# Performance work log

Hardware: AMD Instinct MI355X
Metric: run time of the kernel (lower is better)

## Reference

```python
import jax, jax.numpy as jnp
import numpy as np

NUM_HEADS = 8

def _ln(x, w, b, eps=1e-5):
    m = x.mean(-1, keepdims=True)
    v = ((x - m) ** 2).mean(-1, keepdims=True)
    return (x - m) / jnp.sqrt(v + eps) * w + b

def _l2n(x, axis=-1, eps=1e-12):
    n = jnp.linalg.norm(x, axis=axis, keepdims=True)
    return x / jnp.maximum(n, eps)

def setup_inputs() -> dict:
    key = jax.random.key(0)
    ks = jax.random.split(key, 30)
    B, N, C, nc, t = 2, 4096, 256, 150, 3
    Hh = Ww = 64
    hid = 4 * C
    s = 0.02
    inp = {}
    inp['x'] = jax.random.normal(ks[0], (B, N, C), jnp.float32)
    inp['z'] = jax.random.normal(ks[1], (B, nc, (t + 1) * N), jnp.float32)
    inp['mem'] = jax.random.normal(ks[2], (B * t, N, C), jnp.float32)
    inp['clustering_w'] = s * jax.random.normal(ks[3], (nc, C), jnp.float32)
    inp['prompt1'] = jax.random.normal(ks[4], (nc,), jnp.float32)
    inp['tdt1'] = jnp.eye(nc, dtype=jnp.float32) + s * jax.random.normal(ks[5], (nc, nc), jnp.float32)
    inp['prompt2'] = jax.random.normal(ks[6], (nc,), jnp.float32)
    inp['tdt2'] = jnp.eye(nc, dtype=jnp.float32) + s * jax.random.normal(ks[7], (nc, nc), jnp.float32)
    inp['sim_alpha'] = jnp.ones((1,), jnp.float32)
    inp['sim_beta'] = jnp.zeros((1,), jnp.float32)
    inp['q_w'] = s * jax.random.normal(ks[8], (C, C), jnp.float32)
    inp['q_b'] = s * jax.random.normal(ks[9], (C,), jnp.float32)
    inp['k_w'] = s * jax.random.normal(ks[10], (C, C), jnp.float32)
    inp['k_b'] = s * jax.random.normal(ks[11], (C,), jnp.float32)
    inp['v_w'] = s * jax.random.normal(ks[12], (C, C), jnp.float32)
    inp['v_b'] = s * jax.random.normal(ks[13], (C,), jnp.float32)
    inp['proj_w'] = s * jax.random.normal(ks[14], (C, C), jnp.float32)
    inp['proj_b'] = s * jax.random.normal(ks[15], (C,), jnp.float32)
    inp['norm_w'] = jnp.ones((C,), jnp.float32)
    inp['norm_b'] = jnp.zeros((C,), jnp.float32)
    inp['fc1_w'] = s * jax.random.normal(ks[16], (hid, C), jnp.float32)
    inp['fc1_b'] = s * jax.random.normal(ks[17], (hid,), jnp.float32)
    inp['dw_w'] = s * jax.random.normal(ks[18], (hid, 1, 3, 3), jnp.float32)
    inp['dw_b'] = s * jax.random.normal(ks[19], (hid,), jnp.float32)
    inp['fc2_w'] = s * jax.random.normal(ks[20], (C, hid), jnp.float32)
    inp['fc2_b'] = s * jax.random.normal(ks[21], (C,), jnp.float32)
    inp['H'] = Hh
    inp['W'] = Ww
    inp['t'] = t
    return inp

def _forward(x, z, mem, clustering_w, prompt1, tdt1, prompt2, tdt2, sim_alpha, sim_beta,
             q_w, q_b, k_w, k_b, v_w, v_b, proj_w, proj_b, norm_w, norm_b,
             fc1_w, fc1_b, dw_w, dw_b, fc2_w, fc2_b, H, W, t):
    B, N, C = x.shape
    nc = clustering_w.shape[0]
    res = x
    T = t + 1
    # cat memory frames with current frame: [(B*T), N, C]
    xf = jnp.concatenate([mem.reshape(B, t, N, C), x[:, None]], axis=1).reshape(B * T, N, C)
    # clustering head: (SRPS approximated as identity) 1x1 conv dim->num_clusters
    cl = jnp.einsum('bnc,kc->bkn', xf, clustering_w)            # [(B*T), nc, N]
    cl = cl.reshape(B, T, nc, N).transpose(0, 2, 1, 3).reshape(B, nc, T * N)
    # top-down prompt modulation of z and cluster logits
    zc = z.transpose(0, 2, 1)                                   # [B, T*N, nc]
    cos = _l2n(zc, -1) @ _l2n(prompt1[None, :, None], axis=1)   # [B, T*N, 1]
    zc = (zc * jnp.clip(cos, 0.0, 1.0)) @ tdt1
    clc = cl.transpose(0, 2, 1)
    cos = _l2n(clc, -1) @ _l2n(prompt2[None, :, None], axis=1)
    clc = (clc * jnp.clip(cos, 0.0, 1.0)) @ tdt2
    cluster_x_z = ((clc + zc) * 0.5).transpose(0, 2, 1)          # [B, nc, T*N]
    # inner_center: per-frame soft assignment -> cluster centers
    center = cluster_x_z.reshape(B, nc, T, N).transpose(0, 2, 1, 3)  # [B, T, nc, N]
    assigned_results = center
    soft = jax.nn.softmax(center, axis=-1)
    cx = xf.reshape(B, T, N, C)
    cen = jnp.einsum('btkn,btnc->btkc', soft, cx)               # [B, T, nc, C]
    last, prev = cen[:, -1], cen[:, :-1]                        # [B,nc,C], [B,t,nc,C]
    dot = jnp.einsum('bkc,btkc->btk', last, prev)
    denom = jnp.maximum(jnp.linalg.norm(last, axis=-1)[:, None] * jnp.linalg.norm(prev, axis=-1), 1e-8)
    gate = jax.nn.sigmoid(sim_beta + sim_alpha * (dot / denom))  # [B, t, nc]
    C_in = last + (gate[..., None] * prev).sum(axis=1)          # [B, nc, C]
    C_in = _ln(C_in, norm_w, norm_b)
    # cross attention: tokens query cluster centers
    hd = C // NUM_HEADS
    q = (res @ q_w.T + q_b) * (1.0 / np.sqrt(hd))
    k = C_in @ k_w.T + k_b
    v = C_in @ v_w.T + v_b
    q = q.reshape(B, N, NUM_HEADS, hd).transpose(0, 2, 1, 3)
    k = k.reshape(B, nc, NUM_HEADS, hd).transpose(0, 2, 1, 3)
    v = v.reshape(B, nc, NUM_HEADS, hd).transpose(0, 2, 1, 3)
    attn = jax.nn.softmax(jnp.einsum('bhnd,bhkd->bhnk', q, k), axis=-1)
    o = jnp.einsum('bhnk,bhkd->bhnd', attn, v).transpose(0, 2, 1, 3).reshape(B, N, C)
    o = o @ proj_w.T + proj_b
    out = res + _ln(o, norm_w, norm_b)
    # MLP with depthwise conv
    h = out @ fc1_w.T + fc1_b                                   # [B, N, 4C]
    hid = h.shape[-1]
    h_img = h.transpose(0, 2, 1).reshape(B, hid, H, W)
    h_img = jax.lax.conv_general_dilated(h_img, dw_w, (1, 1), 'SAME',
                                         feature_group_count=hid,
                                         dimension_numbers=('NCHW', 'OIHW', 'NCHW'))
    h_img = h_img + dw_b[None, :, None, None]
    h = h_img.reshape(B, hid, N).transpose(0, 2, 1)
    h = jax.nn.gelu(h, approximate=False) @ fc2_w.T + fc2_b
    out = out + _ln(h, norm_w, norm_b)
    return out, cluster_x_z, assigned_results

def reference(x, z, mem, clustering_w, prompt1, tdt1, prompt2, tdt2, sim_alpha, sim_beta,
              q_w, q_b, k_w, k_b, v_w, v_b, proj_w, proj_b, norm_w, norm_b,
              fc1_w, fc1_b, dw_w, dw_b, fc2_w, fc2_b, H, W, t):
    return _forward(x, z, mem, clustering_w, prompt1, tdt1, prompt2, tdt2, sim_alpha, sim_beta,
                    q_w, q_b, k_w, k_b, v_w, v_b, proj_w, proj_b, norm_w, norm_b,
                    fc1_w, fc1_b, dw_w, dw_b, fc2_w, fc2_b, H, W, t)
```

## Files before the change

### kernel.cpp

```cpp
#include <hip/hip_runtime.h>
#include <math.h>


typedef __attribute__((ext_vector_type(8))) short bf16x8;
typedef __attribute__((ext_vector_type(4))) float f32x4;

__device__ __forceinline__ short f2b(float f) {
  union { float f; unsigned int u; } c; c.f = f;
  unsigned int r = (c.u + 0x7fffu + ((c.u >> 16) & 1u)) >> 16;
  return (short)r;
}

__device__ __forceinline__ float bred_sum(float v, float* red) {
  int tid = threadIdx.x;
  red[tid] = v; __syncthreads();
  #pragma unroll
  for (int s = 128; s > 0; s >>= 1) {
    if (tid < s) red[tid] += red[tid + s];
    __syncthreads();
  }
  float r = red[0]; __syncthreads();
  return r;
}

__global__ __launch_bounds__(256) void gemm_mfma(
    const float* __restrict__ A, const float* __restrict__ W,
    const float* __restrict__ bias, float* __restrict__ out,
    int M, int N, int K, float alpha)
{
  __shared__ __align__(16) short As[128 * 72];
  __shared__ __align__(16) short Bs[64 * 72];
  const int tid = threadIdx.x;
  const int m0 = blockIdx.x * 128;
  const int n0 = blockIdx.y * 64;
  const int wave = tid >> 6;
  const int lane = tid & 63;
  const int wm = wave & 1, wn = wave >> 1;
  const int t16 = lane & 15;
  const int k8 = (lane >> 4) * 8;

  f32x4 acc[4][2];
  #pragma unroll
  for (int i = 0; i < 4; ++i)
    #pragma unroll
    for (int j = 0; j < 2; ++j)
      acc[i][j] = (f32x4){0.f, 0.f, 0.f, 0.f};

  const int sr = tid >> 2;
  const int sk = (tid & 3) * 16;

  for (int k0 = 0; k0 < K; k0 += 64) {
    #pragma unroll
    for (int p = 0; p < 2; ++p) {
      const int row = sr + p * 64;
      const float* ap = &A[(size_t)(m0 + row) * K + k0 + sk];
      float4 v0 = *(const float4*)&ap[0];
      float4 v1 = *(const float4*)&ap[4];
      float4 v2 = *(const float4*)&ap[8];
      float4 v3 = *(const float4*)&ap[12];
      bf16x8 w0, w1;
      w0[0] = f2b(v0.x); w0[1] = f2b(v0.y); w0[2] = f2b(v0.z); w0[3] = f2b(v0.w);
      w0[4] = f2b(v1.x); w0[5] = f2b(v1.y); w0[6] = f2b(v1.z); w0[7] = f2b(v1.w);
      w1[0] = f2b(v2.x); w1[1] = f2b(v2.y); w1[2] = f2b(v2.z); w1[3] = f2b(v2.w);
      w1[4] = f2b(v3.x); w1[5] = f2b(v3.y); w1[6] = f2b(v3.z); w1[7] = f2b(v3.w);
      *(bf16x8*)&As[row * 72 + sk] = w0;
      *(bf16x8*)&As[row * 72 + sk + 8] = w1;
    }
    {
      const float* wp = &W[(size_t)(n0 + sr) * K + k0 + sk];
      float4 v0 = *(const float4*)&wp[0];
      float4 v1 = *(const float4*)&wp[4];
      float4 v2 = *(const float4*)&wp[8];
      float4 v3 = *(const float4*)&wp[12];
      bf16x8 w0, w1;
      w0[0] = f2b(v0.x); w0[1] = f2b(v0.y); w0[2] = f2b(v0.z); w0[3] = f2b(v0.w);
      w0[4] = f2b(v1.x); w0[5] = f2b(v1.y); w0[6] = f2b(v1.z); w0[7] = f2b(v1.w);
      w1[0] = f2b(v2.x); w1[1] = f2b(v2.y); w1[2] = f2b(v2.z); w1[3] = f2b(v2.w);
      w1[4] = f2b(v3.x); w1[5] = f2b(v3.y); w1[6] = f2b(v3.z); w1[7] = f2b(v3.w);
      *(bf16x8*)&Bs[sr * 72 + sk] = w0;
      *(bf16x8*)&Bs[sr * 72 + sk + 8] = w1;
    }
    __syncthreads();
    #pragma unroll
    for (int ks = 0; ks < 2; ++ks) {
      const int kofs = ks * 32 + k8;
      bf16x8 af0 = *(const bf16x8*)&As[(wm * 64 +  0 + t16) * 72 + kofs];
      bf16x8 af1 = *(const bf16x8*)&As[(wm * 64 + 16 + t16) * 72 + kofs];
      bf16x8 af2 = *(const bf16x8*)&As[(wm * 64 + 32 + t16) * 72 + kofs];
      bf16x8 af3 = *(const bf16x8*)&As[(wm * 64 + 48 + t16) * 72 + kofs];
      bf16x8 bf0 = *(const bf16x8*)&Bs[(wn * 32 +  0 + t16) * 72 + kofs];
      bf16x8 bf1 = *(const bf16x8*)&Bs[(wn * 32 + 16 + t16) * 72 + kofs];
      acc[0][0] = __builtin_amdgcn_mfma_f32_16x16x32_bf16(af0, bf0, acc[0][0], 0, 0, 0);
      acc[1][0] = __builtin_amdgcn_mfma_f32_16x16x32_bf16(af1, bf0, acc[1][0], 0, 0, 0);
      acc[2][0] = __builtin_amdgcn_mfma_f32_16x16x32_bf16(af2, bf0, acc[2][0], 0, 0, 0);
      acc[3][0] = __builtin_amdgcn_mfma_f32_16x16x32_bf16(af3, bf0, acc[3][0], 0, 0, 0);
      acc[0][1] = __builtin_amdgcn_mfma_f32_16x16x32_bf16(af0, bf1, acc[0][1], 0, 0, 0);
      acc[1][1] = __builtin_amdgcn_mfma_f32_16x16x32_bf16(af1, bf1, acc[1][1], 0, 0, 0);
      acc[2][1] = __builtin_amdgcn_mfma_f32_16x16x32_bf16(af2, bf1, acc[2][1], 0, 0, 0);
      acc[3][1] = __builtin_amdgcn_mfma_f32_16x16x32_bf16(af3, bf1, acc[3][1], 0, 0, 0);
    }
    __syncthreads();
  }
  const int r4 = (lane >> 4) * 4;
  #pragma unroll
  for (int ni = 0; ni < 2; ++ni) {
    const int gcol = n0 + wn * 32 + ni * 16 + t16;
    const float bb = bias[gcol];
    #pragma unroll
    for (int mi = 0; mi < 4; ++mi) {
      #pragma unroll
      for (int r = 0; r < 4; ++r) {
        const int gm = m0 + wm * 64 + mi * 16 + r4 + r;
        out[(size_t)gm * N + gcol] = alpha * (acc[mi][ni][r] + bb);
      }
    }
  }
}

__global__ __launch_bounds__(256) void gemm_cl_mfma(
    const float* __restrict__ x, const float* __restrict__ mem,
    const float* __restrict__ cw, float* __restrict__ clr)
{
  __shared__ __align__(16) short As[128 * 72];
  __shared__ __align__(16) short Bs[64 * 72];
  const int tid = threadIdx.x;
  const int m0 = blockIdx.x * 128;
  const int n0 = blockIdx.y * 64;
  const int bt = m0 >> 12;
  const int b = bt >> 2, ti = bt & 3;
  const int nbase = m0 & 4095;
  const float* Abase = (ti < 3) ? (mem + (size_t)(b * 3 + ti) * 4096 * 256)
                                : (x + (size_t)b * 4096 * 256);
  const int wave = tid >> 6, lane = tid & 63;
  const int wm = wave & 1, wn = wave >> 1;
  const int t16 = lane & 15;
  const int k8 = (lane >> 4) * 8;

  f32x4 acc[4][2];
  #pragma unroll
  for (int i = 0; i < 4; ++i)
    #pragma unroll
    for (int j = 0; j < 2; ++j)
      acc[i][j] = (f32x4){0.f, 0.f, 0.f, 0.f};

  const int sr = tid >> 2;
  const int sk = (tid & 3) * 16;

  for (int k0 = 0; k0 < 256; k0 += 64) {
    #pragma unroll
    for (int p = 0; p < 2; ++p) {
      const int row = sr + p * 64;
      const float* ap = &Abase[(size_t)(nbase + row) * 256 + k0 + sk];
      float4 v0 = *(const float4*)&ap[0];
      float4 v1 = *(const float4*)&ap[4];
      float4 v2 = *(const float4*)&ap[8];
      float4 v3 = *(const float4*)&ap[12];
      bf16x8 w0, w1;
      w0[0] = f2b(v0.x); w0[1] = f2b(v0.y); w0[2] = f2b(v0.z); w0[3] = f2b(v0.w);
      w0[4] = f2b(v1.x); w0[5] = f2b(v1.y); w0[6] = f2b(v1.z); w0[7] = f2b(v1.w);
      w1[0] = f2b(v2.x); w1[1] = f2b(v2.y); w1[2] = f2b(v2.z); w1[3] = f2b(v2.w);
      w1[4] = f2b(v3.x); w1[5] = f2b(v3.y); w1[6] = f2b(v3.z); w1[7] = f2b(v3.w);
      *(bf16x8*)&As[row * 72 + sk] = w0;
      *(bf16x8*)&As[row * 72 + sk + 8] = w1;
    }
    {
      const int gn = n0 + sr;
      bf16x8 w0 = {0,0,0,0,0,0,0,0}, w1 = {0,0,0,0,0,0,0,0};
      if (gn < 150) {
        const float* wp = &cw[(size_t)gn * 256 + k0 + sk];
        float4 v0 = *(const float4*)&wp[0];
        float4 v1 = *(const float4*)&wp[4];
        float4 v2 = *(const float4*)&wp[8];
        float4 v3 = *(const float4*)&wp[12];
        w0[0] = f2b(v0.x); w0[1] = f2b(v0.y); w0[2] = f2b(v0.z); w0[3] = f2b(v0.w);
        w0[4] = f2b(v1.x); w0[5] = f2b(v1.y); w0[6] = f2b(v1.z); w0[7] = f2b(v1.w);
        w1[0] = f2b(v2.x); w1[1] = f2b(v2.y); w1[2] = f2b(v2.z); w1[3] = f2b(v2.w);
        w1[4] = f2b(v3.x); w1[5] = f2b(v3.y); w1[6] = f2b(v3.z); w1[7] = f2b(v3.w);
      }
      *(bf16x8*)&Bs[sr * 72 + sk] = w0;
      *(bf16x8*)&Bs[sr * 72 + sk + 8] = w1;
    }
    __syncthreads();
    #pragma unroll
    for (int ks = 0; ks < 2; ++ks) {
      const int kofs = ks * 32 + k8;
      bf16x8 af0 = *(const bf16x8*)&As[(wm * 64 +  0 + t16) * 72 + kofs];
      bf16x8 af1 = *(const bf16x8*)&As[(wm * 64 + 16 + t16) * 72 + kofs];
      bf16x8 af2 = *(const bf16x8*)&As[(wm * 64 + 32 + t16) * 72 + kofs];
      bf16x8 af3 = *(const bf16x8*)&As[(wm * 64 + 48 + t16) * 72 + kofs];
      bf16x8 bf0 = *(const bf16x8*)&Bs[(wn * 32 +  0 + t16) * 72 + kofs];
      bf16x8 bf1 = *(const bf16x8*)&Bs[(wn * 32 + 16 + t16) * 72 + kofs];
      acc[0][0] = __builtin_amdgcn_mfma_f32_16x16x32_bf16(af0, bf0, acc[0][0], 0, 0, 0);
      acc[1][0] = __builtin_amdgcn_mfma_f32_16x16x32_bf16(af1, bf0, acc[1][0], 0, 0, 0);
      acc[2][0] = __builtin_amdgcn_mfma_f32_16x16x32_bf16(af2, bf0, acc[2][0], 0, 0, 0);
      acc[3][0] = __builtin_amdgcn_mfma_f32_16x16x32_bf16(af3, bf0, acc[3][0], 0, 0, 0);
      acc[0][1] = __builtin_amdgcn_mfma_f32_16x16x32_bf16(af0, bf1, acc[0][1], 0, 0, 0);
      acc[1][1] = __builtin_amdgcn_mfma_f32_16x16x32_bf16(af1, bf1, acc[1][1], 0, 0, 0);
      acc[2][1] = __builtin_amdgcn_mfma_f32_16x16x32_bf16(af2, bf1, acc[2][1], 0, 0, 0);
      acc[3][1] = __builtin_amdgcn_mfma_f32_16x16x32_bf16(af3, bf1, acc[3][1], 0, 0, 0);
    }
    __syncthreads();
  }
  const int r4 = (lane >> 4) * 4;
  const size_t rowbase = (size_t)b * 16384 + ti * 4096 + nbase;
  #pragma unroll
  for (int ni = 0; ni < 2; ++ni) {
    const int col = n0 + wn * 32 + ni * 16 + t16;
    if (col >= 160) continue;
    #pragma unroll
    for (int mi = 0; mi < 4; ++mi) {
      const int mrow = wm * 64 + mi * 16 + r4;
      #pragma unroll
      for (int r = 0; r < 4; ++r)
        clr[(rowbase + mrow + r) * 160 + col] = acc[mi][ni][r];
    }
  }
}

__global__ __launch_bounds__(256) void cos_stats(
    const float* __restrict__ z, const float* __restrict__ clr,
    const float* __restrict__ p1, const float* __restrict__ p2,
    float* __restrict__ cosz, float* __restrict__ coscl)
{
  int which = blockIdx.y;
  int gid = blockIdx.x * 256 + threadIdx.x;
  int b = gid >> 14, m = gid & 16383;
  float d = 0, s = 0, pn = 0;
  if (which) {
    const float* sp = clr + ((size_t)b * 16384 + m) * 160;
    for (int k = 0; k < 148; k += 4) {
      float4 v = *(const float4*)&sp[k];
      float4 a = *(const float4*)&p2[k];
      d += v.x * a.x + v.y * a.y + v.z * a.z + v.w * a.w;
      s += v.x * v.x + v.y * v.y + v.z * v.z + v.w * v.w;
      pn += a.x * a.x + a.y * a.y + a.z * a.z + a.w * a.w;
    }
    for (int k = 148; k < 150; ++k) {
      float v = sp[k], a = p2[k];
      d += v * a; s += v * v; pn += a * a;
    }
    float c = d / (fmaxf(sqrtf(s), 1e-12f) * fmaxf(sqrtf(pn), 1e-12f));
    coscl[gid] = fminf(fmaxf(c, 0.f), 1.f);
  } else {
    const float* sp = z + (size_t)b * 150 * 16384 + m;
    for (int k = 0; k < 150; ++k) {
      float v = sp[(size_t)k * 16384];
      float a = p1[k];
      d += v * a; s += v * v; pn += a * a;
    }
    float c = d / (fmaxf(sqrtf(s), 1e-12f) * fmaxf(sqrtf(pn), 1e-12f));
    cosz[gid] = fminf(fmaxf(c, 0.f), 1.f);
  }
}

__global__ __launch_bounds__(256) void gemm_csz_mfma(
    const float* __restrict__ clr, const float* __restrict__ z,
    const float* __restrict__ coscl, const float* __restrict__ cosz,
    const float* __restrict__ tdt2, const float* __restrict__ tdt1,
    float* __restrict__ csz, float* __restrict__ asg)
{
  __shared__ __align__(16) short As[128 * 40];
  __shared__ __align__(16) short Bs[64 * 40];
  const int tid = threadIdx.x;
  const int m0 = blockIdx.x * 128;
  const int b = m0 >> 14;
  const int mm = m0 & 16383;
  const int n0 = blockIdx.y * 64;
  const int wave = tid >> 6, lane = tid & 63;
  const int wm = wave & 1, wn = wave >> 1;
  const int t16 = lane & 15;
  const int k8 = (lane >> 4) * 8;

  f32x4 acc[4][2];
  #pragma unroll
  for (int i = 0; i < 4; ++i)
    #pragma unroll
    for (int j = 0; j < 2; ++j)
      acc[i][j] = (f32x4){0.f, 0.f, 0.f, 0.f};

  for (int c = 0; c < 10; ++c) {
    if (c < 5) {
      const int row = tid >> 1;
      const int sk0 = (tid & 1) * 16;
      const float* ap = &clr[((size_t)b * 16384 + mm + row) * 160 + c * 32 + sk0];
      const float cs = coscl[(size_t)b * 16384 + mm + row];
      float4 v0 = *(const float4*)&ap[0];
      float4 v1 = *(const float4*)&ap[4];
      float4 v2 = *(const float4*)&ap[8];
      float4 v3 = *(const float4*)&ap[12];
      bf16x8 w0, w1;
      w0[0] = f2b(v0.x * cs); w0[1] = f2b(v0.y * cs); w0[2] = f2b(v0.z * cs); w0[3] = f2b(v0.w * cs);
      w0[4] = f2b(v1.x * cs); w0[5] = f2b(v1.y * cs); w0[6] = f2b(v1.z * cs); w0[7] = f2b(v1.w * cs);
      w1[0] = f2b(v2.x * cs); w1[1] = f2b(v2.y * cs); w1[2] = f2b(v2.z * cs); w1[3] = f2b(v2.w * cs);
      w1[4] = f2b(v3.x * cs); w1[5] = f2b(v3.y * cs); w1[6] = f2b(v3.z * cs); w1[7] = f2b(v3.w * cs);
      *(bf16x8*)&As[row * 40 + sk0] = w0;
      *(bf16x8*)&As[row * 40 + sk0 + 8] = w1;
    } else {
      const int kgl = tid >> 3;
      const int mb = (tid & 7) * 4;
      const int kg = (c - 5) * 32 + kgl;
      #pragma unroll
      for (int p = 0; p < 4; ++p) {
        const int m = mb + p * 32;
        float4 v = make_float4(0.f, 0.f, 0.f, 0.f);
        if (kg < 150) {
          v = *(const float4*)&z[((size_t)b * 150 + kg) * 16384 + mm + m];
          float4 cz = *(const float4*)&cosz[(size_t)b * 16384 + mm + m];
          v.x *= cz.x; v.y *= cz.y; v.z *= cz.z; v.w *= cz.w;
        }
        As[(m + 0) * 40 + kgl] = f2b(v.x);
        As[(m + 1) * 40 + kgl] = f2b(v.y);
        As[(m + 2) * 40 + kgl] = f2b(v.z);
        As[(m + 3) * 40 + kgl] = f2b(v.w);
      }
    }
    {
      const int kc = tid & 63;
      const int gn = n0 + kc;
      #pragma unroll
      for (int p = 0; p < 8; ++p) {
        const int kgl = (tid >> 6) + p * 4;
        const int kg = c * 32 + kgl;
        float t = 0.f;
        if (gn < 150) {
          if (kg < 150) t = tdt2[kg * 150 + gn];
          else if (kg >= 160 && kg < 310) t = tdt1[(kg - 160) * 150 + gn];
        }
        Bs[kc * 40 + kgl] = f2b(t);
      }
    }
    __syncthreads();
    {
      bf16x8 af0 = *(const bf16x8*)&As[(wm * 64 +  0 + t16) * 40 + k8];
      bf16x8 af1 = *(const bf16x8*)&As[(wm * 64 + 16 + t16) * 40 + k8];
      bf16x8 af2 = *(const bf16x8*)&As[(wm * 64 + 32 + t16) * 40 + k8];
      bf16x8 af3 = *(const bf16x8*)&As[(wm * 64 + 48 + t16) * 40 + k8];
      bf16x8 bf0 = *(const bf16x8*)&Bs[(wn * 32 +  0 + t16) * 40 + k8];
      bf16x8 bf1 = *(const bf16x8*)&Bs[(wn * 32 + 16 + t16) * 40 + k8];
      acc[0][0] = __builtin_amdgcn_mfma_f32_16x16x32_bf16(af0, bf0, acc[0][0], 0, 0, 0);
      acc[1][0] = __builtin_amdgcn_mfma_f32_16x16x32_bf16(af1, bf0, acc[1][0], 0, 0, 0);
      acc[2][0] = __builtin_amdgcn_mfma_f32_16x16x32_bf16(af2, bf0, acc[2][0], 0, 0, 0);
      acc[3][0] = __builtin_amdgcn_mfma_f32_16x16x32_bf16(af3, bf0, acc[3][0], 0, 0, 0);
      acc[0][1] = __builtin_amdgcn_mfma_f32_16x16x32_bf16(af0, bf1, acc[0][1], 0, 0, 0);
      acc[1][1] = __builtin_amdgcn_mfma_f32_16x16x32_bf16(af1, bf1, acc[1][1], 0, 0, 0);
      acc[2][1] = __builtin_amdgcn_mfma_f32_16x16x32_bf16(af2, bf1, acc[2][1], 0, 0, 0);
      acc[3][1] = __builtin_amdgcn_mfma_f32_16x16x32_bf16(af3, bf1, acc[3][1], 0, 0, 0);
    }
    __syncthreads();
  }
  const int r4 = (lane >> 4) * 4;
  const int ti = mm >> 12;
  const int nn = mm & 4095;
  #pragma unroll
  for (int ni = 0; ni < 2; ++ni) {
    const int kc = n0 + wn * 32 + ni * 16 + t16;
    if (kc >= 150) continue;
    #pragma unroll
    for (int mi = 0; mi < 4; ++mi) {
      const int mrow = wm * 64 + mi * 16 + r4;
      float4 r;
      r.x = 0.5f * acc[mi][ni][0];
      r.y = 0.5f * acc[mi][ni][1];
      r.z = 0.5f * acc[mi][ni][2];
      r.w = 0.5f * acc[mi][ni][3];
      *(float4*)&csz[((size_t)b * 150 + kc) * 16384 + mm + mrow] = r;
      *(float4*)&asg[(((size_t)b * 4 + ti) * 150 + kc) * 4096 + nn + mrow] = r;
    }
  }
}

__global__ __launch_bounds__(256) void softmax_stats_e(
    const float* __restrict__ csz, float* __restrict__ lr_, short* __restrict__ ecsz)
{
  __shared__ float wred[8];
  const int row = blockIdx.x;
  const int bt = row / 150, k = row - bt * 150;
  const int b = bt >> 2, ti = bt & 3;
  const float* p = csz + ((size_t)b * 150 + k) * 16384 + ti * 4096;
  const int base = threadIdx.x * 16;
  float4 v[4];
  #pragma unroll
  for (int i = 0; i < 4; ++i) v[i] = *(const float4*)&p[base + i * 4];
  float mx = -1e30f;
  #pragma unroll
  for (int i = 0; i < 4; ++i)
    mx = fmaxf(mx, fmaxf(fmaxf(v[i].x, v[i].y), fmaxf(v[i].z, v[i].w)));
  #pragma unroll
  for (int off = 1; off < 64; off <<= 1) mx = fmaxf(mx, __shfl_xor(mx, off));
  const int wave = threadIdx.x >> 6, lane = threadIdx.x & 63;
  if (lane == 0) wred[wave] = mx;
  __syncthreads();
  mx = fmaxf(fmaxf(wred[0], wred[1]), fmaxf(wred[2], wred[3]));
  const float L = 1.4426950408889634f;
  float s = 0.f;
  bf16x8 e0, e1;
  #pragma unroll
  for (int i = 0; i < 2; ++i) {
    float a = exp2f((v[i].x - mx) * L);
    float bq = exp2f((v[i].y - mx) * L);
    float cq = exp2f((v[i].z - mx) * L);
    float dq = exp2f((v[i].w - mx) * L);
    s += a + bq + cq + dq;
    e0[i * 4 + 0] = f2b(a); e0[i * 4 + 1] = f2b(bq); e0[i * 4 + 2] = f2b(cq); e0[i * 4 + 3] = f2b(dq);
  }
  #pragma unroll
  for (int i = 2; i < 4; ++i) {
    float a = exp2f((v[i].x - mx) * L);
    float bq = exp2f((v[i].y - mx) * L);
    float cq = exp2f((v[i].z - mx) * L);
    float dq = exp2f((v[i].w - mx) * L);
    s += a + bq + cq + dq;
    e1[(i - 2) * 4 + 0] = f2b(a); e1[(i - 2) * 4 + 1] = f2b(bq);
    e1[(i - 2) * 4 + 2] = f2b(cq); e1[(i - 2) * 4 + 3] = f2b(dq);
  }
  #pragma unroll
  for (int off = 1; off < 64; off <<= 1) s += __shfl_xor(s, off);
  if (lane == 0) wred[4 + wave] = s;
  __syncthreads();
  short* er = ecsz + ((size_t)bt * 160 + k) * 4096 + base;
  *(bf16x8*)&er[0] = e0;
  *(bf16x8*)&er[8] = e1;
  if (threadIdx.x == 0) lr_[row] = wred[4] + wred[5] + wred[6] + wred[7];
}

__global__ __launch_bounds__(256) void gemm_cen_at(
    const short* __restrict__ ecsz, const float* __restrict__ x, const float* __restrict__ mem,
    float* __restrict__ cen)
{
  __shared__ __align__(16) short As[160 * 136];
  const int tid = threadIdx.x;
  const int chalf = blockIdx.x;
  const int bt = blockIdx.y;
  const int sp = blockIdx.z;
  const int b = bt >> 2, ti = bt & 3;
  const float* xf = (ti < 3) ? (mem + (size_t)(b * 3 + ti) * 4096 * 256)
                             : (x + (size_t)b * 4096 * 256);
  const int n0 = sp * 256;
  const int wave = tid >> 6, lane = tid & 63;
  const int t16 = lane & 15, quad = lane >> 4, k8 = quad * 8;
  const int cbase = chalf * 128 + wave * 32;

  f32x4 acc[10][2];
  #pragma unroll
  for (int i = 0; i < 10; ++i) {
    acc[i][0] = (f32x4){0.f, 0.f, 0.f, 0.f};
    acc[i][1] = (f32x4){0.f, 0.f, 0.f, 0.f};
  }

  const short* erow = ecsz + (size_t)bt * 160 * 4096 + n0;
  #pragma unroll
  for (int half = 0; half < 2; ++half) {
    #pragma unroll
    for (int p = 0; p < 10; ++p) {
      const int g = p * 256 + tid;
      const int row = g >> 4;
      const int col8 = (g & 15) * 8;
      *(bf16x8*)&As[row * 136 + col8] =
          *(const bf16x8*)&erow[(size_t)row * 4096 + half * 128 + col8];
    }
    __syncthreads();
    #pragma unroll
    for (int kc = 0; kc < 4; ++kc) {
      bf16x8 bB[2];
      #pragma unroll
      for (int nt = 0; nt < 2; ++nt) {
        bf16x8 w;
        #pragma unroll
        for (int j = 0; j < 8; ++j)
          w[j] = f2b(xf[(size_t)(n0 + half * 128 + kc * 32 + k8 + j) * 256 + cbase + nt * 16 + t16]);
        bB[nt] = w;
      }
      #pragma unroll
      for (int mt = 0; mt < 10; ++mt) {
        bf16x8 aA = *(const bf16x8*)&As[(mt * 16 + t16) * 136 + kc * 32 + k8];
        acc[mt][0] = __builtin_amdgcn_mfma_f32_16x16x32_bf16(aA, bB[0], acc[mt][0], 0, 0, 0);
        acc[mt][1] = __builtin_amdgcn_mfma_f32_16x16x32_bf16(aA, bB[1], acc[mt][1], 0, 0, 0);
      }
    }
    __syncthreads();
  }
  #pragma unroll
  for (int mt = 0; mt < 10; ++mt) {
    #pragma unroll
    for (int r = 0; r < 4; ++r) {
      const int grow = mt * 16 + quad * 4 + r;
      if (grow < 150) {
        atomicAdd(&cen[((size_t)bt * 150 + grow) * 256 + cbase + t16], acc[mt][0][r]);
        atomicAdd(&cen[((size_t)bt * 150 + grow) * 256 + cbase + 16 + t16], acc[mt][1][r]);
      }
    }
  }
}

__global__ __launch_bounds__(256) void gate_ln(
    const float* __restrict__ cen, const float* __restrict__ lr_,
    const float* __restrict__ alpha_, const float* __restrict__ beta_,
    const float* __restrict__ nw, const float* __restrict__ nb, float* __restrict__ cin)
{
  __shared__ float red[256];
  int bk = blockIdx.x;
  int b = bk / 150, k = bk % 150;
  int c = threadIdx.x;
  const float* base = cen + ((size_t)b * 4 * 150) * 256;
  const float* lrb = lr_ + (size_t)b * 4 * 150;
  float lc  = base[((size_t)3 * 150 + k) * 256 + c] / lrb[3 * 150 + k];
  float p0  = base[((size_t)0 * 150 + k) * 256 + c] / lrb[0 * 150 + k];
  float p1v = base[((size_t)1 * 150 + k) * 256 + c] / lrb[1 * 150 + k];
  float p2v = base[((size_t)2 * 150 + k) * 256 + c] / lrb[2 * 150 + k];
  float nl = bred_sum(lc * lc, red);
  float q0 = bred_sum(p0 * p0, red);
  float q1 = bred_sum(p1v * p1v, red);
  float q2 = bred_sum(p2v * p2v, red);
  float d0 = bred_sum(lc * p0, red);
  float d1 = bred_sum(lc * p1v, red);
  float d2 = bred_sum(lc * p2v, red);
  float al = alpha_[0], be = beta_[0];
  float snl = sqrtf(nl);
  float g0 = 1.f / (1.f + expf(-(be + al * (d0 / fmaxf(snl * sqrtf(q0), 1e-8f)))));
  float g1 = 1.f / (1.f + expf(-(be + al * (d1 / fmaxf(snl * sqrtf(q1), 1e-8f)))));
// ... 149 lines not shown
      ls += __shfl_xor(ls, 4);
      ls += __shfl_xor(ls, 8);
      if (t16 == 0) lrow[wr + mt * 16 + quad * 4 + r] = 1.f / ls;
      #pragma unroll
      for (int ct = 0; ct < 10; ++ct)
        Ps[(wr + mt * 16 + quad * 4 + r) * 168 + ct * 16 + t16] = f2b(s[mt][ct][r]);
    }
  }
  __syncthreads();

  f32x4 oacc[2][2];
  #pragma unroll
  for (int i = 0; i < 2; ++i)
    #pragma unroll
    for (int j = 0; j < 2; ++j)
      oacc[i][j] = (f32x4){0.f, 0.f, 0.f, 0.f};
  #pragma unroll
  for (int kstep = 0; kstep < 5; ++kstep) {
    bf16x8 bV0 = *(const bf16x8*)&VT[( 0 + t16) * 168 + kstep * 32 + k8];
    bf16x8 bV1 = *(const bf16x8*)&VT[(16 + t16) * 168 + kstep * 32 + k8];
    #pragma unroll
    for (int mt = 0; mt < 2; ++mt) {
      bf16x8 aP = *(const bf16x8*)&Ps[(wr + mt * 16 + t16) * 168 + kstep * 32 + k8];
      oacc[mt][0] = __builtin_amdgcn_mfma_f32_16x16x32_bf16(aP, bV0, oacc[mt][0], 0, 0, 0);
      oacc[mt][1] = __builtin_amdgcn_mfma_f32_16x16x32_bf16(aP, bV1, oacc[mt][1], 0, 0, 0);
    }
  }
  #pragma unroll
  for (int mt = 0; mt < 2; ++mt) {
    #pragma unroll
    for (int nt = 0; nt < 2; ++nt) {
      const int d = nt * 16 + t16;
      #pragma unroll
      for (int r = 0; r < 4; ++r) {
        const int row = wr + mt * 16 + quad * 4 + r;
        o[((size_t)b * 4096 + n0 + row) * 256 + h * 32 + d] = oacc[mt][nt][r] * lrow[row];
      }
    }
  }
}

__global__ __launch_bounds__(256) void ln_res(
    const float* __restrict__ src, const float* __restrict__ res,
    const float* __restrict__ nw, const float* __restrict__ nb, float* __restrict__ dst)
{
  const int wave = threadIdx.x >> 6;
  const int lane = threadIdx.x & 63;
  const size_t row = (size_t)blockIdx.x * 4 + wave;
  const int c = lane * 4;
  float4 v = *(const float4*)&src[row * 256 + c];
  float s  = v.x + v.y + v.z + v.w;
  float s2 = v.x * v.x + v.y * v.y + v.z * v.z + v.w * v.w;
  #pragma unroll
  for (int off = 1; off < 64; off <<= 1) {
    s  += __shfl_xor(s, off);
    s2 += __shfl_xor(s2, off);
  }
  const float mu = s * (1.f / 256.f);
  const float var = s2 * (1.f / 256.f) - mu * mu;
  const float inv = rsqrtf(var + 1e-5f);
  float4 w = *(const float4*)&nw[c];
  float4 bb = *(const float4*)&nb[c];
  float4 rr = *(const float4*)&res[row * 256 + c];
  float4 d;
  d.x = rr.x + (v.x - mu) * inv * w.x + bb.x;
  d.y = rr.y + (v.y - mu) * inv * w.y + bb.y;
  d.z = rr.z + (v.z - mu) * inv * w.z + bb.z;
  d.w = rr.w + (v.w - mu) * inv * w.w + bb.w;
  *(float4*)&dst[row * 256 + c] = d;
}

__global__ __launch_bounds__(256) void conv_wt(
    const float* __restrict__ w, float* __restrict__ wt)
{
  int i = blockIdx.x * 256 + threadIdx.x;
  if (i < 9216) {
    int ch = i / 9, tap = i - ch * 9;
    wt[tap * 1024 + ch] = w[i];
  }
}

__global__ __launch_bounds__(256) void conv_gelu(
    const float* __restrict__ h, const float* __restrict__ wt, const float* __restrict__ bias,
    float* __restrict__ hc)
{
  const int pix = blockIdx.x;
  const int b = pix >> 12;
  const int n = pix & 4095;
  const int y = n >> 6, xx = n & 63;
  const int c4 = threadIdx.x * 4;
  float4 acc = *(const float4*)&bias[c4];
  const float* hb = h + ((size_t)b * 4096) * 1024 + c4;
  #pragma unroll
  for (int dy = 0; dy < 3; ++dy) {
    const int yy = y + dy - 1;
    if (yy < 0 || yy > 63) continue;
    #pragma unroll
    for (int dx = 0; dx < 3; ++dx) {
      const int xv = xx + dx - 1;
      if (xv < 0 || xv > 63) continue;
      float4 hv = *(const float4*)&hb[(size_t)(yy * 64 + xv) * 1024];
      float4 wv = *(const float4*)&wt[(dy * 3 + dx) * 1024 + c4];
      acc.x = fmaf(hv.x, wv.x, acc.x);
      acc.y = fmaf(hv.y, wv.y, acc.y);
      acc.z = fmaf(hv.z, wv.z, acc.z);
      acc.w = fmaf(hv.w, wv.w, acc.w);
    }
  }
  float4 g;
  g.x = 0.5f * acc.x * (1.f + erff(acc.x * 0.70710678118654752f));
  g.y = 0.5f * acc.y * (1.f + erff(acc.y * 0.70710678118654752f));
  g.z = 0.5f * acc.z * (1.f + erff(acc.z * 0.70710678118654752f));
  g.w = 0.5f * acc.w * (1.f + erff(acc.w * 0.70710678118654752f));
  *(float4*)&hc[((size_t)b * 4096 + n) * 1024 + c4] = g;
}

extern "C" void kernel_launch(void* const* d_in, const int* in_sizes, int n_in,
                              void* d_out, int out_size, void* d_ws, size_t ws_size,
                              hipStream_t stream)
{
  (void)in_sizes; (void)n_in; (void)out_size; (void)ws_size;
  const float* x    = (const float*)d_in[0];
  const float* z    = (const float*)d_in[1];
  const float* mem  = (const float*)d_in[2];
  const float* cw   = (const float*)d_in[3];
  const float* p1   = (const float*)d_in[4];
  const float* tdt1 = (const float*)d_in[5];
  const float* p2   = (const float*)d_in[6];
  const float* tdt2 = (const float*)d_in[7];
  const float* sal  = (const float*)d_in[8];
  const float* sbe  = (const float*)d_in[9];
  const float* q_w  = (const float*)d_in[10];
  const float* q_b  = (const float*)d_in[11];
  const float* k_w  = (const float*)d_in[12];
  const float* k_b  = (const float*)d_in[13];
  const float* v_w  = (const float*)d_in[14];
  const float* v_b  = (const float*)d_in[15];
  const float* pj_w = (const float*)d_in[16];
  const float* pj_b = (const float*)d_in[17];
  const float* nw   = (const float*)d_in[18];
  const float* nb   = (const float*)d_in[19];
  const float* f1w  = (const float*)d_in[20];
  const float* f1b  = (const float*)d_in[21];
  const float* dww  = (const float*)d_in[22];
  const float* dwb  = (const float*)d_in[23];
  const float* f2w  = (const float*)d_in[24];
  const float* f2b_ = (const float*)d_in[25];

  float* out = (float*)d_out;
  float* csz = out + 2097152;
  float* asg = csz + 4915200;

  float* ws    = (float*)d_ws;
  float* clr   = ws;
  short* ecsz  = (short*)ws;
  float* coscl = ws + 5242880;
  float* cosz  = ws + 5275648;
  float* lr_   = ws + 5308416;
  float* cen   = ws + 5310816;
  float* cin   = ws + 5618016;
  float* q     = ws + 5694816;
  float* ksb   = ws + 7791968;
  float* vsb   = ws + 7868768;
  float* o     = ws + 7945568;
  float* h     = ws;
  float* hc    = ws + 8388608;
  float* tmp   = ws + 16777216;
  float* out1  = ws + 18874368;
  float* wt    = ws + 20971520;

  dim3 blk(256);
  gemm_cl_mfma<<<dim3(256, 3), blk, 0, stream>>>(x, mem, cw, clr);
  cos_stats<<<dim3(128, 2), blk, 0, stream>>>(z, clr, p1, p2, cosz, coscl);
  gemm_csz_mfma<<<dim3(256, 3), blk, 0, stream>>>(clr, z, coscl, cosz, tdt2, tdt1, csz, asg);
  softmax_stats_e<<<dim3(1200), blk, 0, stream>>>(csz, lr_, ecsz);
  hipMemsetAsync(cen, 0, (size_t)1200 * 256 * sizeof(float), stream);
  gemm_cen_at<<<dim3(2, 8, 16), blk, 0, stream>>>(ecsz, x, mem, cen);
  gate_ln<<<dim3(300), blk, 0, stream>>>(cen, lr_, sal, sbe, nw, nb, cin);
  gemm_mfma<<<dim3(64, 4), blk, 0, stream>>>(x, q_w, q_b, q, 8192, 256, 256, 0.17677669529663687f);
  gemm_nt<<<dim3(3, 4), blk, 0, stream>>>(cin, k_w, k_b, ksb, 300, 256, 256, 1.f);
  gemm_nt<<<dim3(3, 4), blk, 0, stream>>>(cin, v_w, v_b, vsb, 300, 256, 256, 1.f);
  attn_mfma<<<dim3(512), blk, 0, stream>>>(q, ksb, vsb, o);
  gemm_mfma<<<dim3(64, 4), blk, 0, stream>>>(o, pj_w, pj_b, tmp, 8192, 256, 256, 1.f);
  ln_res<<<dim3(2048), blk, 0, stream>>>(tmp, x, nw, nb, out1);
  gemm_mfma<<<dim3(64, 16), blk, 0, stream>>>(out1, f1w, f1b, h, 8192, 1024, 256, 1.f);
  conv_wt<<<dim3(36), blk, 0, stream>>>(dww, wt);
  conv_gelu<<<dim3(8192), blk, 0, stream>>>(h, wt, dwb, hc);
  gemm_mfma<<<dim3(64, 4), blk, 0, stream>>>(hc, f2w, f2b_, tmp, 8192, 256, 1024, 1.f);
  ln_res<<<dim3(2048), blk, 0, stream>>>(tmp, out1, nw, nb, out);
}
```

Measured before the change: 447.9 us.

## Fuse clustering GEMM with cosine gating into a bf16 concatenated operand

After: 445.5 us. No clear change (-0.5%).

```diff
diff --git a/kernel.cpp b/kernel.cpp
--- a/kernel.cpp
+++ b/kernel.cpp
@@ -117,254 +117,227 @@
   }
 }
 
-__global__ __launch_bounds__(256) void gemm_cl_mfma(
+__global__ __launch_bounds__(256) void prep_bt(
+    const float* __restrict__ cw, const float* __restrict__ tdt2, const float* __restrict__ tdt1,
+    short* __restrict__ cwb, short* __restrict__ TT)
+{
+  int idx = blockIdx.x * 256 + threadIdx.x;
+  if (idx < 160 * 256) {
+    int kc = idx >> 8, k = idx & 255;
+    float v = (kc < 150) ? cw[kc * 256 + k] : 0.f;
+    cwb[idx] = f2b(v);
+  }
+  if (idx < 160 * 320) {
+    int kc = idx / 320, kk = idx - kc * 320;
+    float t = 0.f;
+    if (kc < 150) {
+      if (kk < 150) t = tdt2[kk * 150 + kc];
+      else if (kk >= 160 && kk < 310) t = tdt1[(kk - 160) * 150 + kc];
+    }
+    TT[idx] = f2b(t);
+  }
+}
+
+__global__ __launch_bounds__(256) void cl_cos_prep(
     const float* __restrict__ x, const float* __restrict__ mem,
-    const float* __restrict__ cw, float* __restrict__ clr)
-{
-  __shared__ __align__(16) short As[128 * 72];
-  __shared__ __align__(16) short Bs[64 * 72];
+    const short* __restrict__ cwb, const float* __restrict__ p2,
+    short* __restrict__ Acat)
+{
+  __shared__ __align__(16) short ls[64][168];
+  __shared__ float p2s[160];
   const int tid = threadIdx.x;
-  const int m0 = blockIdx.x * 128;
-  const int n0 = blockIdx.y * 64;
-  const int bt = m0 >> 12;
-  const int b = bt >> 2, ti = bt & 3;
-  const int nbase = m0 & 4095;
-  const float* Abase = (ti < 3) ? (mem + (size_t)(b * 3 + ti) * 4096 * 256)
-                                : (x + (size_t)b * 4096 * 256);
+  const int r0 = blockIdx.x * 64;
+  const int b = r0 >> 14, ti = (r0 >> 12) & 3;
+  const int nn0 = r0 & 4095;
+  const float* Ab = ((ti < 3) ? (mem + (size_t)(b * 3 + ti) * 4096 * 256)
+                              : (x + (size_t)b * 4096 * 256)) + (size_t)nn0 * 256;
+  const int wave = tid >> 6, lane = tid & 63;
+  const int t16 = lane & 15, quad = lane >> 4, k8 = quad * 8;
+  if (tid < 160) p2s[tid] = (tid < 150) ? p2[tid] : 0.f;
+  __syncthreads();
+
+  f32x4 acc[10];
+  #pragma unroll
+  for (int i = 0; i < 10; ++i) acc[i] = (f32x4){0.f, 0.f, 0.f, 0.f};
+  const float* ap = Ab + (size_t)(wave * 16 + t16) * 256 + k8;
+  const short* bp = cwb + t16 * 256 + k8;
+  #pragma unroll 2
+  for (int ks = 0; ks < 8; ++ks) {
+    float4 v0 = *(const float4*)&ap[ks * 32];
+    float4 v1 = *(const float4*)&ap[ks * 32 + 4];
+    bf16x8 a;
+    a[0] = f2b(v0.x); a[1] = f2b(v0.y); a[2] = f2b(v0.z); a[3] = f2b(v0.w);
+    a[4] = f2b(v1.x); a[5] = f2b(v1.y); a[6] = f2b(v1.z); a[7] = f2b(v1.w);
+    #pragma unroll
+    for (int nf = 0; nf < 10; ++nf) {
+      bf16x8 bv = *(const bf16x8*)&bp[nf * 4096 + ks * 32];
+      acc[nf] = __builtin_amdgcn_mfma_f32_16x16x32_bf16(a, bv, acc[nf], 0, 0, 0);
+    }
+  }
+  float d[4] = {0.f, 0.f, 0.f, 0.f}, s[4] = {0.f, 0.f, 0.f, 0.f};
+  float pn = 0.f;
+  #pragma unroll
+  for (int nf = 0; nf < 10; ++nf) {
+    float a2 = p2s[nf * 16 + t16];
+    pn += a2 * a2;
+    #pragma unroll
+    for (int r = 0; r < 4; ++r) {
+      float v = acc[nf][r];
+      d[r] = fmaf(v, a2, d[r]);
+      s[r] = fmaf(v, v, s[r]);
+    }
+  }
+  #pragma unroll
+  for (int off = 1; off < 16; off <<= 1) {
+    pn += __shfl_xor(pn, off);
+    #pragma unroll
+    for (int r = 0; r < 4; ++r) {
+      d[r] += __shfl_xor(d[r], off);
+      s[r] += __shfl_xor(s[r], off);
+    }
+  }
+  const float spn = fmaxf(sqrtf(pn), 1e-12f);
+  float cs[4];
+  #pragma unroll
+  for (int r = 0; r < 4; ++r) {
+    float c = d[r] / (fmaxf(sqrtf(s[r]), 1e-12f) * spn);
+    cs[r] = fminf(fmaxf(c, 0.f), 1.f);
+  }
+  #pragma unroll
+  for (int nf = 0; nf < 10; ++nf)
+    #pragma unroll
+    for (int r = 0; r < 4; ++r)
+      ls[wave * 16 + quad * 4 + r][nf * 16 + t16] = f2b(acc[nf][r] * cs[r]);
+  __syncthreads();
+  #pragma unroll
+  for (int i = 0; i < 5; ++i) {
+    const int idx = tid + i * 256;
+    const int m = idx / 20, seg = idx - m * 20;
+    *(bf16x8*)&Acat[(size_t)(r0 + m) * 320 + seg * 8] = *(const bf16x8*)&ls[m][seg * 8];
+  }
+}
+
+__global__ __launch_bounds__(256) void z_prep(
+    const float* __restrict__ z, const float* __restrict__ p1, short* __restrict__ Acat)
+{
+  __shared__ __align__(16) float zs[160][68];
+  __shared__ float sred[4][16][9];
+  __shared__ float czs[64];
+  const int tid = threadIdx.x;
+  const int C0 = blockIdx.x * 64;
+  const int b = C0 >> 14;
+  const int mmb = C0 & 16383;
+  const int kr = tid >> 4, c4 = (tid & 15) * 4;
+  float d[4] = {0.f, 0.f, 0.f, 0.f}, sv[4] = {0.f, 0.f, 0.f, 0.f};
+  float pn = 0.f;
+  #pragma unroll
+  for (int it = 0; it < 10; ++it) {
+    const int k = it * 16 + kr;
+    float4 v = make_float4(0.f, 0.f, 0.f, 0.f);
+    float a = 0.f;
+    if (k < 150) {
+      v = *(const float4*)&z[((size_t)b * 150 + k) * 16384 + mmb + c4];
+      a = p1[k];
+    }
+    *(float4*)&zs[k][c4] = v;
+    d[0] = fmaf(v.x, a, d[0]); d[1] = fmaf(v.y, a, d[1]);
+    d[2] = fmaf(v.z, a, d[2]); d[3] = fmaf(v.w, a, d[3]);
+    sv[0] = fmaf(v.x, v.x, sv[0]); sv[1] = fmaf(v.y, v.y, sv[1]);
+    sv[2] = fmaf(v.z, v.z, sv[2]); sv[3] = fmaf(v.w, v.w, sv[3]);
+    pn = fmaf(a, a, pn);
+  }
+  const int lane = tid & 63, wave = tid >> 6;
+  #pragma unroll
+  for (int off = 16; off < 64; off <<= 1) {
+    pn += __shfl_xor(pn, off);
+    #pragma unroll
+    for (int r = 0; r < 4; ++r) {
+      d[r] += __shfl_xor(d[r], off);
+      sv[r] += __shfl_xor(sv[r], off);
+    }
+  }
+  if ((lane >> 4) == 0) {
+    #pragma unroll
+    for (int r = 0; r < 4; ++r) {
+      sred[wave][lane][r] = d[r];
+      sred[wave][lane][4 + r] = sv[r];
+    }
+    sred[wave][lane][8] = pn;
+  }
+  __syncthreads();
+  if (tid < 64) {
+    const int cg = tid >> 2, r = tid & 3;
+    float dd = 0.f, ss = 0.f, pp = 0.f;
+    #pragma unroll
+    for (int w = 0; w < 4; ++w) {
+      dd += sred[w][cg][r];
+      ss += sred[w][cg][4 + r];
+      pp += sred[w][cg][8];
+    }
+    float c = dd / (fmaxf(sqrtf(ss), 1e-12f) * fmaxf(sqrtf(pp), 1e-12f));
+    czs[tid] = fminf(fmaxf(c, 0.f), 1.f);
+  }
+  __syncthreads();
+  #pragma unroll
+  for (int i = 0; i < 5; ++i) {
+    const int idx = tid + i * 256;
+    const int m = idx / 20, seg = idx - m * 20;
+    const float cz = czs[m];
+    bf16x8 w;
+    #pragma unroll
+    for (int j = 0; j < 8; ++j) w[j] = f2b(zs[seg * 8 + j][m] * cz);
+    *(bf16x8*)&Acat[(size_t)(C0 + m) * 320 + 160 + seg * 8] = w;
+  }
+}
+
+__global__ __launch_bounds__(256) void gemm_csz2(
+    const short* __restrict__ Acat, const short* __restrict__ TT,
+    float* __restrict__ csz, float* __restrict__ asg)
+{
+  const int tid = threadIdx.x;
+  const int r0 = blockIdx.x * 64;
+  const int b = r0 >> 14;
+  const int mmg = r0 & 16383;
+  const int ti = mmg >> 12, nn = mmg & 4095;
   const int wave = tid >> 6, lane = tid & 63;
   const int wm = wave & 1, wn = wave >> 1;
-  const int t16 = lane & 15;
-  const int k8 = (lane >> 4) * 8;
-
-  f32x4 acc[4][2];
-  #pragma unroll
-  for (int i = 0; i < 4; ++i)
-    #pragma unroll
-    for (int j = 0; j < 2; ++j)
+  const int t16 = lane & 15, quad = lane >> 4, k8 = quad * 8;
+  f32x4 acc[2][5];
+  #pragma unroll
+  for (int i = 0; i < 2; ++i)
+    #pragma unroll
+    for (int j = 0; j < 5; ++j)
       acc[i][j] = (f32x4){0.f, 0.f, 0.f, 0.f};
 
-  const int sr = tid >> 2;
-  const int sk = (tid & 3) * 16;
-
-  for (int k0 = 0; k0 < 256; k0 += 64) {
-    #pragma unroll
-    for (int p = 0; p < 2; ++p) {
-      const int row = sr + p * 64;
-      const float* ap = &Abase[(size_t)(nbase + row) * 256 + k0 + sk];
-      float4 v0 = *(const float4*)&ap[0];
-      float4 v1 = *(const float4*)&ap[4];
-      float4 v2 = *(const float4*)&ap[8];
-      float4 v3 = *(const float4*)&ap[12];
-      bf16x8 w0, w1;
-      w0[0] = f2b(v0.x); w0[1] = f2b(v0.y); w0[2] = f2b(v0.z); w0[3] = f2b(v0.w);
-      w0[4] = f2b(v1.x); w0[5] = f2b(v1.y); w0[6] = f2b(v1.z); w0[7] = f2b(v1.w);
-      w1[0] = f2b(v2.x); w1[1] = f2b(v2.y); w1[2] = f2b(v2.z); w1[3] = f2b(v2.w);
-      w1[4] = f2b(v3.x); w1[5] = f2b(v3.y); w1[6] = f2b(v3.z); w1[7] = f2b(v3.w);
-      *(bf16x8*)&As[row * 72 + sk] = w0;
-      *(bf16x8*)&As[row * 72 + sk + 8] = w1;
-    }
-    {
-      const int gn = n0 + sr;
-      bf16x8 w0 = {0,0,0,0,0,0,0,0}, w1 = {0,0,0,0,0,0,0,0};
-      if (gn < 150) {
-        const float* wp = &cw[(size_t)gn * 256 + k0 + sk];
-        float4 v0 = *(const float4*)&wp[0];
-        float4 v1 = *(const float4*)&wp[4];
-        float4 v2 = *(const float4*)&wp[8];
-        float4 v3 = *(const float4*)&wp[12];
-        w0[0] = f2b(v0.x); w0[1] = f2b(v0.y); w0[2] = f2b(v0.z); w0[3] = f2b(v0.w);
-        w0[4] = f2b(v1.x); w0[5] = f2b(v1.y); w0[6] = f2b(v1.z); w0[7] = f2b(v1.w);
-        w1[0] = f2b(v2.x); w1[1] = f2b(v2.y); w1[2] = f2b(v2.z); w1[3] = f2b(v2.w);
-        w1[4] = f2b(v3.x); w1[5] = f2b(v3.y); w1[6] = f2b(v3.z); w1[7] = f2b(v3.w);
+  const short* a0p = Acat + (size_t)(r0 + wm * 32 + t16) * 320 + k8;
+  const short* a1p = a0p + 16 * 320;
+  const short* bp  = TT + (size_t)(wn * 80 + t16) * 320 + k8;
+  #pragma unroll 2
+  for (int ks = 0; ks < 10; ++ks) {
+    bf16x8 a0 = *(const bf16x8*)&a0p[ks * 32];
+    bf16x8 a1 = *(const bf16x8*)&a1p[ks * 32];
+    #pragma unroll
+    for (int nf = 0; nf < 5; ++nf) {
+      bf16x8 bv = *(const bf16x8*)&bp[nf * 5120 + ks * 32];
+      acc[0][nf] = __builtin_amdgcn_mfma_f32_16x16x32_bf16(a0, bv, acc[0][nf], 0, 0, 0);
+      acc[1][nf] = __builtin_amdgcn_mfma_f32_16x16x32_bf16(a1, bv, acc[1][nf], 0, 0, 0);
+    }
+  }
+  #pragma unroll
+  for (int nf = 0; nf < 5; ++nf) {
+    const int kc = wn * 80 + nf * 16 + t16;
+    if (kc < 150) {
+      #pragma unroll
+      for (int mf = 0; mf < 2; ++mf) {
+        const int moff = wm * 32 + mf * 16 + quad * 4;
+        float4 r4;
+        r4.x = 0.5f * acc[mf][nf][0];
+        r4.y = 0.5f * acc[mf][nf][1];
+        r4.z = 0.5f * acc[mf][nf][2];
+        r4.w = 0.5f * acc[mf][nf][3];
+        *(float4*)&csz[((size_t)b * 150 + kc) * 16384 + mmg + moff] = r4;
+        *(float4*)&asg[(((size_t)b * 4 + ti) * 150 + kc) * 4096 + nn + moff] = r4;
       }
-      *(bf16x8*)&Bs[sr * 72 + sk] = w0;
-      *(bf16x8*)&Bs[sr * 72 + sk + 8] = w1;
-    }
-    __syncthreads();
-    #pragma unroll
-    for (int ks = 0; ks < 2; ++ks) {
-      const int kofs = ks * 32 + k8;
-      bf16x8 af0 = *(const bf16x8*)&As[(wm * 64 +  0 + t16) * 72 + kofs];
-      bf16x8 af1 = *(const bf16x8*)&As[(wm * 64 + 16 + t16) * 72 + kofs];
-      bf16x8 af2 = *(const bf16x8*)&As[(wm * 64 + 32 + t16) * 72 + kofs];
-      bf16x8 af3 = *(const bf16x8*)&As[(wm * 64 + 48 + t16) * 72 + kofs];
-      bf16x8 bf0 = *(const bf16x8*)&Bs[(wn * 32 +  0 + t16) * 72 + kofs];
-      bf16x8 bf1 = *(const bf16x8*)&Bs[(wn * 32 + 16 + t16) * 72 + kofs];
-      acc[0][0] = __builtin_amdgcn_mfma_f32_16x16x32_bf16(af0, bf0, acc[0][0], 0, 0, 0);
-      acc[1][0] = __builtin_amdgcn_mfma_f32_16x16x32_bf16(af1, bf0, acc[1][0], 0, 0, 0);
-      acc[2][0] = __builtin_amdgcn_mfma_f32_16x16x32_bf16(af2, bf0, acc[2][0], 0, 0, 0);
-      acc[3][0] = __builtin_amdgcn_mfma_f32_16x16x32_bf16(af3, bf0, acc[3][0], 0, 0, 0);
-      acc[0][1] = __builtin_amdgcn_mfma_f32_16x16x32_bf16(af0, bf1, acc[0][1], 0, 0, 0);
-      acc[1][1] = __builtin_amdgcn_mfma_f32_16x16x32_bf16(af1, bf1, acc[1][1], 0, 0, 0);
-      acc[2][1] = __builtin_amdgcn_mfma_f32_16x16x32_bf16(af2, bf1, acc[2][1], 0, 0, 0);
-      acc[3][1] = __builtin_amdgcn_mfma_f32_16x16x32_bf16(af3, bf1, acc[3][1], 0, 0, 0);
-    }
-    __syncthreads();
-  }
-  const int r4 = (lane >> 4) * 4;
-  const size_t rowbase = (size_t)b * 16384 + ti * 4096 + nbase;
-  #pragma unroll
-  for (int ni = 0; ni < 2; ++ni) {
-    const int col = n0 + wn * 32 + ni * 16 + t16;
-    if (col >= 160) continue;
-    #pragma unroll
-    for (int mi = 0; mi < 4; ++mi) {
-      const int mrow = wm * 64 + mi * 16 + r4;
-      #pragma unroll
-      for (int r = 0; r < 4; ++r)
-        clr[(rowbase + mrow + r) * 160 + col] = acc[mi][ni][r];
-    }
-  }
-}
-
-__global__ __launch_bounds__(256) void cos_stats(
-    const float* __restrict__ z, const float* __restrict__ clr,
-    const float* __restrict__ p1, const float* __restrict__ p2,
-    float* __restrict__ cosz, float* __restrict__ coscl)
-{
-  int which = blockIdx.y;
-  int gid = blockIdx.x * 256 + threadIdx.x;
-  int b = gid >> 14, m = gid & 16383;
-  float d = 0, s = 0, pn = 0;
-  if (which) {
-    const float* sp = clr + ((size_t)b * 16384 + m) * 160;
-    for (int k = 0; k < 148; k += 4) {
-      float4 v = *(const float4*)&sp[k];
-      float4 a = *(const float4*)&p2[k];
-      d += v.x * a.x + v.y * a.y + v.z * a.z + v.w * a.w;
-      s += v.x * v.x + v.y * v.y + v.z * v.z + v.w * v.w;
-      pn += a.x * a.x + a.y * a.y + a.z * a.z + a.w * a.w;
-    }
-    for (int k = 148; k < 150; ++k) {
-      float v = sp[k], a = p2[k];
-      d += v * a; s += v * v; pn += a * a;
-    }
-    float c = d / (fmaxf(sqrtf(s), 1e-12f) * fmaxf(sqrtf(pn), 1e-12f));
-    coscl[gid] = fminf(fmaxf(c, 0.f), 1.f);
-  } else {
-    const float* sp = z + (size_t)b * 150 * 16384 + m;
-    for (int k = 0; k < 150; ++k) {
-      float v = sp[(size_t)k * 16384];
-      float a = p1[k];
-      d += v * a; s += v * v; pn += a * a;
-    }
-    float c = d / (fmaxf(sqrtf(s), 1e-12f) * fmaxf(sqrtf(pn), 1e-12f));
-    cosz[gid] = fminf(fmaxf(c, 0.f), 1.f);
-  }
-}
-
-__global__ __launch_bounds__(256) void gemm_csz_mfma(
-    const float* __restrict__ clr, const float* __restrict__ z,
-    const float* __restrict__ coscl, const float* __restrict__ cosz,
-    const float* __restrict__ tdt2, const float* __restrict__ tdt1,
-    float* __restrict__ csz, float* __restrict__ asg)
-{
-  __shared__ __align__(16) short As[128 * 40];
-  __shared__ __align__(16) short Bs[64 * 40];
-  const int tid = threadIdx.x;
-  const int m0 = blockIdx.x * 128;
-  const int b = m0 >> 14;
-  const int mm = m0 & 16383;
-  const int n0 = blockIdx.y * 64;
-  const int wave = tid >> 6, lane = tid & 63;
-  const int wm = wave & 1, wn = wave >> 1;
-  const int t16 = lane & 15;
-  const int k8 = (lane >> 4) * 8;
-
-  f32x4 acc[4][2];
-  #pragma unroll
-  for (int i = 0; i < 4; ++i)
-    #pragma unroll
-    for (int j = 0; j < 2; ++j)
-      acc[i][j] = (f32x4){0.f, 0.f, 0.f, 0.f};
-
-  for (int c = 0; c < 10; ++c) {
-    if (c < 5) {
-      const int row = tid >> 1;
-      const int sk0 = (tid & 1) * 16;
-      const float* ap = &clr[((size_t)b * 16384 + mm + row) * 160 + c * 32 + sk0];
-      const float cs = coscl[(size_t)b * 16384 + mm + row];
-      float4 v0 = *(const float4*)&ap[0];
-      float4 v1 = *(const float4*)&ap[4];
-      float4 v2 = *(const float4*)&ap[8];
-      float4 v3 = *(const float4*)&ap[12];
-      bf16x8 w0, w1;
-      w0[0] = f2b(v0.x * cs); w0[1] = f2b(v0.y * cs); w0[2] = f2b(v0.z * cs); w0[3] = f2b(v0.w * cs);
-      w0[4] = f2b(v1.x * cs); w0[5] = f2b(v1.y * cs); w0[6] = f2b(v1.z * cs); w0[7] = f2b(v1.w * cs);
-      w1[0] = f2b(v2.x * cs); w1[1] = f2b(v2.y * cs); w1[2] = f2b(v2.z * cs); w1[3] = f2b(v2.w * cs);
-      w1[4] = f2b(v3.x * cs); w1[5] = f2b(v3.y * cs); w1[6] = f2b(v3.z * cs); w1[7] = f2b(v3.w * cs);
-      *(bf16x8*)&As[row * 40 + sk0] = w0;
-      *(bf16x8*)&As[row * 40 + sk0 + 8] = w1;
-    } else {
-      const int kgl = tid >> 3;
-      const int mb = (tid & 7) * 4;
-      const int kg = (c - 5) * 32 + kgl;
-      #pragma unroll
-      for (int p = 0; p < 4; ++p) {
-        const int m = mb + p * 32;
-        float4 v = make_float4(0.f, 0.f, 0.f, 0.f);
-        if (kg < 150) {
-          v = *(const float4*)&z[((size_t)b * 150 + kg) * 16384 + mm + m];
-          float4 cz = *(const float4*)&cosz[(size_t)b * 16384 + mm + m];
-          v.x *= cz.x; v.y *= cz.y; v.z *= cz.z; v.w *= cz.w;
-        }
-        As[(m + 0) * 40 + kgl] = f2b(v.x);
-        As[(m + 1) * 40 + kgl] = f2b(v.y);
-        As[(m + 2) * 40 + kgl] = f2b(v.z);
-        As[(m + 3) * 40 + kgl] = f2b(v.w);
-      }
-    }
-    {
-      const int kc = tid & 63;
-      const int gn = n0 + kc;
-      #pragma unroll
-      for (int p = 0; p < 8; ++p) {
-        const int kgl = (tid >> 6) + p * 4;
-        const int kg = c * 32 + kgl;
-        float t = 0.f;
-        if (gn < 150) {
-          if (kg < 150) t = tdt2[kg * 150 + gn];
-          else if (kg >= 160 && kg < 310) t = tdt1[(kg - 160) * 150 + gn];
-        }
-        Bs[kc * 40 + kgl] = f2b(t);
-      }
-    }
-    __syncthreads();
-    {
-      bf16x8 af0 = *(const bf16x8*)&As[(wm * 64 +  0 + t16) * 40 + k8];
-      bf16x8 af1 = *(const bf16x8*)&As[(wm * 64 + 16 + t16) * 40 + k8];
-      bf16x8 af2 = *(const bf16x8*)&As[(wm * 64 + 32 + t16) * 40 + k8];
-      bf16x8 af3 = *(const bf16x8*)&As[(wm * 64 + 48 + t16) * 40 + k8];
-      bf16x8 bf0 = *(const bf16x8*)&Bs[(wn * 32 +  0 + t16) * 40 + k8];
-      bf16x8 bf1 = *(const bf16x8*)&Bs[(wn * 32 + 16 + t16) * 40 + k8];
-      acc[0][0] = __builtin_amdgcn_mfma_f32_16x16x32_bf16(af0, bf0, acc[0][0], 0, 0, 0);
-      acc[1][0] = __builtin_amdgcn_mfma_f32_16x16x32_bf16(af1, bf0, acc[1][0], 0, 0, 0);
-      acc[2][0] = __builtin_amdgcn_mfma_f32_16x16x32_bf16(af2, bf0, acc[2][0], 0, 0, 0);
-      acc[3][0] = __builtin_amdgcn_mfma_f32_16x16x32_bf16(af3, bf0, acc[3][0], 0, 0, 0);
-      acc[0][1] = __builtin_amdgcn_mfma_f32_16x16x32_bf16(af0, bf1, acc[0][1], 0, 0, 0);
-      acc[1][1] = __builtin_amdgcn_mfma_f32_16x16x32_bf16(af1, bf1, acc[1][1], 0, 0, 0);
-      acc[2][1] = __builtin_amdgcn_mfma_f32_16x16x32_bf16(af2, bf1, acc[2][1], 0, 0, 0);
-      acc[3][1] = __builtin_amdgcn_mfma_f32_16x16x32_bf16(af3, bf1, acc[3][1], 0, 0, 0);
-    }
-    __syncthreads();
-  }
-  const int r4 = (lane >> 4) * 4;
-  const int ti = mm >> 12;
-  const int nn = mm & 4095;
-  #pragma unroll
-  for (int ni = 0; ni < 2; ++ni) {
-    const int kc = n0 + wn * 32 + ni * 16 + t16;
-    if (kc >= 150) continue;
-    #pragma unroll
-    for (int mi = 0; mi < 4; ++mi) {
-      const int mrow = wm * 64 + mi * 16 + r4;
-      float4 r;
-      r.x = 0.5f * acc[mi][ni][0];
-      r.y = 0.5f * acc[mi][ni][1];
-      r.z = 0.5f * acc[mi][ni][2];
-      r.w = 0.5f * acc[mi][ni][3];
-      *(float4*)&csz[((size_t)b * 150 + kc) * 16384 + mm + mrow] = r;
-      *(float4*)&asg[(((size_t)b * 4 + ti) * 150 + kc) * 4096 + nn + mrow] = r;
     }
   }
 }
@@ -820,10 +793,10 @@
   float* asg = csz + 4915200;
 
   float* ws    = (float*)d_ws;
-  float* clr   = ws;
+  short* Acat  = (short*)ws;
   short* ecsz  = (short*)ws;
-  float* coscl = ws + 5242880;
-  float* cosz  = ws + 5275648;
+  short* TT    = (short*)(ws + 5242880);
+  short* cwb   = (short*)(ws + 5275648);
   float* lr_   = ws + 5308416;
   float* cen   = ws + 5310816;
   float* cin   = ws + 5618016;
@@ -838,9 +811,10 @@
   float* wt    = ws + 20971520;
 
   dim3 blk(256);
-  gemm_cl_mfma<<<dim3(256, 3), blk, 0, stream>>>(x, mem, cw, clr);
-  cos_stats<<<dim3(128, 2), blk, 0, stream>>>(z, clr, p1, p2, cosz, coscl);
-  gemm_csz_mfma<<<dim3(256, 3), blk, 0, stream>>>(clr, z, coscl, cosz, tdt2, tdt1, csz, asg);
+  prep_bt<<<dim3(200), blk, 0, stream>>>(cw, tdt2, tdt1, cwb, TT);
+  z_prep<<<dim3(512), blk, 0, stream>>>(z, p1, Acat);
+  cl_cos_prep<<<dim3(512), blk, 0, stream>>>(x, mem, cwb, p2, Acat);
+  gemm_csz2<<<dim3(512), blk, 0, stream>>>(Acat, TT, csz, asg);
   softmax_stats_e<<<dim3(1200), blk, 0, stream>>>(csz, lr_, ecsz);
   hipMemsetAsync(cen, 0, (size_t)1200 * 256 * sizeof(float), stream);
   gemm_cen_at<<<dim3(2, 8, 16), blk, 0, stream>>>(ecsz, x, mem, cen);
```
